# Kernel optimization log

Hardware: AMD Instinct MI355X
Metric: run time of the kernel (lower is better)

The kernel has to match this reference:

```python
import jax, jax.numpy as jnp
import numpy as np
import itertools

DIM = 7
N_H2, N_H3 = 21, 77

def _perm_sign(p):
    inv = sum(1 for i in range(len(p)) for j in range(i + 1, len(p)) if p[i] > p[j])
    return -1.0 if inv % 2 else 1.0

def _build_wedge_constants():
    # C[a,b,c] = sign of (pair_a, pair_b, triple_c) as a permutation of (0..6),
    # zero unless the 2+2+3 indices are disjoint (coefficient of the volume form
    # in omega_a ^ omega_b ^ Phi_c on ordered-multi-index components).
    idx2 = list(itertools.combinations(range(DIM), 2))   # 21 ordered pairs
    idx3 = list(itertools.combinations(range(DIM), 3))   # 35 ordered triples
    C = np.zeros((len(idx2), len(idx2), len(idx3)), dtype=np.float32)
    for a, pa in enumerate(idx2):
        sa = set(pa)
        for b, pb in enumerate(idx2):
            if sa & set(pb):
                continue
            sab = sa | set(pb)
            for c, pc in enumerate(idx3):
                full = pa + pb + pc
                if sab.isdisjoint(pc):
                    C[a, b, c] = _perm_sign(full)
    return jnp.asarray(C)

C_WEDGE = _build_wedge_constants()  # (21, 21, 35), sparse structure constants

def setup_inputs() -> dict:
    key = jax.random.key(0)
    k1, k2, k3 = jax.random.split(key, 3)
    batch = 4096
    omega = jax.random.normal(k1, (batch, N_H2, 21), dtype=jnp.float32)
    Phi = jax.random.normal(k2, (batch, N_H3, 35), dtype=jnp.float32)
    metric = jax.random.normal(k3, (batch, DIM, DIM), dtype=jnp.float32)
    return {"omega": omega, "Phi": Phi, "metric": metric}

def reference(omega, Phi, metric):
    # Monte-Carlo volume weights, normalized (normalize=True path)
    vol = jnp.sqrt(jnp.abs(jnp.linalg.det(metric)))        # (n,)
    w = vol / vol.sum()
    # Fused triple wedge contraction replacing the 21*21*77 python loops:
    # D[n,i,j,c] = sum_{a,b} C[a,b,c] omega[n,i,a] omega[n,j,b]
    D = jnp.einsum('abc,nia,njb->nijc', C_WEDGE, omega, omega)
    Pw = Phi * w[:, None, None]                             # fold MC weight into Phi
    S = jnp.einsum('nijc,nkc->ijk', D, Pw)                  # (21,21,77), symmetric in i,j
    # Original code writes +integral for j>=i and forces -integral for j<i
    upper = jnp.triu(jnp.ones((N_H2, N_H2), dtype=bool))[:, :, None]
    Y = jnp.where(upper, S, -S)
    # Gram matrix and spectrum
    M = jnp.einsum('ijk,ijl->kl', Y, Y)                     # (77,77)
    eigenvalues = jnp.linalg.eigvalsh(M)[::-1]              # descending, like torch path
    return Y, M, eigenvalues
```

## Files before the change

kernel.cpp:

```cpp
#include <hip/hip_runtime.h>
#include <math.h>

#define NBATCH 4096
#define NH2 21
#define NK 77
#define NC 35
#define NIJ 441
#define Y_SIZE 33957
#define M_SIZE 5929
#define VOLOFF Y_SIZE
#define VSUM (Y_SIZE + 4096)
#define NPAIR 231
#define BLK 512
#define NPB 8
#define GRID_B (NBATCH / NPB)
#define EIGT 640

#define NSLOT 16
#define SLOT_STRIDE 17792
#define WS2OFF (NSLOT * SLOT_STRIDE)

#define SZ_OMEGA  (NBATCH * NH2 * NH2)
#define SZ_PHI    (NBATCH * NK * NC)
#define SZ_METRIC (NBATCH * 7 * 7)

struct WTab {
  int a[NC][6];
  int b[NC][6];
  int sg[NC][6];
};

constexpr WTab make_wtab() {
  WTab W{};
  int p0[21] = {}, p1[21] = {};
  int idx = 0;
  for (int x = 0; x < 7; ++x)
    for (int y = x + 1; y < 7; ++y) { p0[idx] = x; p1[idx] = y; ++idx; }
  int t0[35] = {}, t1[35] = {}, t2[35] = {};
  idx = 0;
  for (int x = 0; x < 7; ++x)
    for (int y = x + 1; y < 7; ++y)
      for (int z = y + 1; z < 7; ++z) { t0[idx] = x; t1[idx] = y; t2[idx] = z; ++idx; }
  int cnt[35] = {};
  for (int a = 0; a < 21; ++a)
    for (int b = 0; b < 21; ++b) {
      int pa0 = p0[a], pa1 = p1[a], pb0 = p0[b], pb1 = p1[b];
      if (pa0 == pb0 || pa0 == pb1 || pa1 == pb0 || pa1 == pb1) continue;
      bool used[7] = {};
      used[pa0] = true; used[pa1] = true; used[pb0] = true; used[pb1] = true;
      int tr[3] = {}; int k = 0;
      for (int x = 0; x < 7; ++x) if (!used[x]) tr[k++] = x;
      int c = -1;
      for (int cc = 0; cc < 35; ++cc)
        if (t0[cc] == tr[0] && t1[cc] == tr[1] && t2[cc] == tr[2]) { c = cc; break; }
      int perm[7] = {pa0, pa1, pb0, pb1, tr[0], tr[1], tr[2]};
      int inv = 0;
      for (int i = 0; i < 7; ++i)
        for (int j = i + 1; j < 7; ++j)
          if (perm[i] > perm[j]) ++inv;
      W.a[c][cnt[c]] = a; W.b[c][cnt[c]] = b; W.sg[c][cnt[c]] = (inv & 1) ? -1 : 1;
      ++cnt[c];
    }
  return W;
}

__device__ __forceinline__ int trioff(int i) { return 21 * i - (i * (i - 1)) / 2; }

__device__ __forceinline__ unsigned f2bf(float x) {
  union { float f; unsigned u; } v; v.f = x;
  return ((v.u + 0x7FFFu + ((v.u >> 16) & 1u)) >> 16) & 0xFFFFu;
}

typedef float f32x4 __attribute__((ext_vector_type(4)));
typedef short s16x8 __attribute__((ext_vector_type(8)));

template <int CTRL>
__device__ __forceinline__ float dppadd(float x) {
  union { float f; int i; } u, r;
  u.f = x;
  r.i = __builtin_amdgcn_update_dpp(0, u.i, CTRL, 0xF, 0xF, true);
  return x + r.f;
}
__device__ __forceinline__ float oct_sum(float x) {
  x = dppadd<0xB1>(x);
  x = dppadd<0x4E>(x);
  x = dppadd<0x141>(x);
  return x;
}
__device__ __forceinline__ float wave_sum(float x) {
  x = dppadd<0xB1>(x);
  x = dppadd<0x4E>(x);
  x = dppadd<0x141>(x);
  x = dppadd<0x140>(x);
  x = dppadd<0x142>(x);
  x = dppadd<0x143>(x);
  return x;
}
__device__ __forceinline__ float readlane63(float x) {
  union { float f; int i; } u; u.f = x;
  union { int i; float f; } r;
  r.i = __builtin_amdgcn_readlane(u.i, 63);
  return r.f;
}

__global__ __launch_bounds__(256) void vol_kernel(const float* __restrict__ metric,
                                                  float* __restrict__ out) {
  const int n = blockIdx.x * 256 + threadIdx.x;
  double a[7][7];
#pragma unroll
  for (int r = 0; r < 7; ++r)
#pragma unroll
    for (int c = 0; c < 7; ++c) a[r][c] = (double)metric[n * 49 + r * 7 + c];

  double det = 1.0;
#pragma unroll
  for (int k = 0; k < 7; ++k) {
#pragma unroll
    for (int r = k + 1; r < 7; ++r) {
      bool sw = fabs(a[r][k]) > fabs(a[k][k]);
#pragma unroll
      for (int c = k; c < 7; ++c) {
        double u = a[k][c], v = a[r][c];
        a[k][c] = sw ? v : u;
        a[r][c] = sw ? u : v;
      }
    }
    det *= a[k][k];
    double inv = (a[k][k] != 0.0) ? 1.0 / a[k][k] : 0.0;
#pragma unroll
    for (int r = k + 1; r < 7; ++r) {
      double f = a[r][k] * inv;
#pragma unroll
      for (int c = k + 1; c < 7; ++c) a[r][c] -= f * a[k][c];
    }
  }
  float vol = (float)sqrt(fabs(det));
  out[VOLOFF + n] = vol;

  float s = vol;
#pragma unroll
  for (int off = 32; off > 0; off >>= 1) s += __shfl_down(s, off, 64);
  __shared__ float partial[4];
  const int lane = threadIdx.x & 63, wv = threadIdx.x >> 6;
  if (lane == 0) partial[wv] = s;
  __syncthreads();
  if (threadIdx.x == 0)
    atomicAdd(out + VSUM, partial[0] + partial[1] + partial[2] + partial[3]);
}

__global__ __launch_bounds__(BLK) void contract_kernel(const float* __restrict__ omega,
                                                       const float* __restrict__ Phi,
                                                       const float* __restrict__ out,
                                                       float* __restrict__ wsS) {
  constexpr WTab W = make_wtab();
  __shared__ __align__(16) short ldsD[256 * 80];
  __shared__ __align__(16) short ldsP[80 * 80];
  __shared__ __align__(16) float ldsO[NH2 * 28];

  const int t = threadIdx.x;
  const int lane = t & 63;
  const int wv = t >> 6;
  const int quad = lane >> 4;
  const int col = lane & 15;
  const int n0 = blockIdx.x * NPB;

  for (int f = t; f < 256 * 40; f += BLK) ((int*)ldsD)[f] = 0;
  for (int f = t; f < 80 * 40; f += BLK) ((int*)ldsP)[f] = 0;

  const bool roleA = (t < NPAIR);
  const bool roleB = (t >= 256) && (t < 256 + NPAIR);
  int pi = 0, pj = 0;
  {
    const int p = roleA ? t : (roleB ? (t - 256) : 0);
    int i = 0;
    while (i < 20 && trioff(i + 1) <= p) ++i;
    pi = i;
    pj = p - trioff(i) + i;
  }

  float rA = 0.0f, rB[6], rvn;
  {
    const float* om = omega + n0 * 441;
    const float* ph = Phi + n0 * 2695;
    if (t < 441) rA = om[t];
#pragma unroll
    for (int j = 0; j < 6; ++j) {
      const int e = t + j * BLK;
      rB[j] = (e < 2695) ? ph[e] : 0.0f;
    }
    rvn = out[VOLOFF + n0];
  }

  f32x4 acc[2][5];
#pragma unroll
  for (int mi = 0; mi < 2; ++mi)
#pragma unroll
    for (int nt = 0; nt < 5; ++nt) acc[mi][nt] = (f32x4){0.f, 0.f, 0.f, 0.f};

  for (int it = 0; it < NPB; ++it) {
    __syncthreads();

    if (t < 441) ldsO[(t / 21) * 28 + (t % 21)] = rA;
    {
      const float vn = rvn;
#pragma unroll
      for (int j = 0; j < 6; ++j) {
        const int e = t + j * BLK;
        if (e < 2695) {
          const int q = e / 35, c = e % 35;
          ldsP[q * 80 + c] = (short)f2bf(vn * rB[j]);
        }
      }
    }
    __syncthreads();

    if (it + 1 < NPB) {
      const int n1 = n0 + it + 1;
      const float* om2 = omega + n1 * 441;
      const float* ph2 = Phi + n1 * 2695;
      if (t < 441) rA = om2[t];
#pragma unroll
      for (int j = 0; j < 6; ++j) {
        const int e = t + j * BLK;
        if (e < 2695) rB[j] = ph2[e];
      }
      rvn = out[VOLOFF + n1];
    }

    if (roleA || roleB) {
      float wi[21], wj[21];
      const float* oi = ldsO + pi * 28;
      const float* oj = ldsO + pj * 28;
#pragma unroll
      for (int a = 0; a < 20; a += 4) {
        float4 v = *(const float4*)(oi + a);
        wi[a] = v.x; wi[a + 1] = v.y; wi[a + 2] = v.z; wi[a + 3] = v.w;
        float4 u = *(const float4*)(oj + a);
        wj[a] = u.x; wj[a + 1] = u.y; wj[a + 2] = u.z; wj[a + 3] = u.w;
      }
      wi[20] = oi[20]; wj[20] = oj[20];

      if (roleA) {
        float d[18];
#pragma unroll
        for (int c = 0; c < 18; ++c) {
          float dd = 0.0f;
#pragma unroll
          for (int u = 0; u < 6; ++u)
            dd = fmaf((W.sg[c][u] > 0) ? wi[W.a[c][u]] : -wi[W.a[c][u]], wj[W.b[c][u]], dd);
          d[c] = dd;
        }
        int* Drow = (int*)ldsD + t * 40;
#pragma unroll
        for (int k2 = 0; k2 < 9; ++k2)
          Drow[k2] = (int)(f2bf(d[2 * k2]) | (f2bf(d[2 * k2 + 1]) << 16));
      } else {
        float d[17];
#pragma unroll
        for (int c = 18; c < 35; ++c) {
          float dd = 0.0f;
#pragma unroll
          for (int u = 0; u < 6; ++u)
            dd = fmaf((W.sg[c][u] > 0) ? wi[W.a[c][u]] : -wi[W.a[c][u]], wj[W.b[c][u]], dd);
          d[c - 18] = dd;
        }
        int* Drow = (int*)ldsD + (t - 256) * 40;
#pragma unroll
        for (int k2 = 0; k2 < 8; ++k2)
          Drow[9 + k2] = (int)(f2bf(d[2 * k2]) | (f2bf(d[2 * k2 + 1]) << 16));
        Drow[17] = (int)f2bf(d[16]);
      }
    }
    __syncthreads();

#pragma unroll
    for (int s = 0; s < 2; ++s) {
      const int kof = s * 32 + quad * 8;
      s16x8 a0 = *(const s16x8*)(ldsD + ((wv * 2 + 0) * 16 + col) * 80 + kof);
      s16x8 a1 = *(const s16x8*)(ldsD + ((wv * 2 + 1) * 16 + col) * 80 + kof);
      s16x8 b[5];
#pragma unroll
      for (int nt = 0; nt < 5; ++nt)
        b[nt] = *(const s16x8*)(ldsP + (nt * 16 + col) * 80 + kof);
#pragma unroll
      for (int nt = 0; nt < 5; ++nt) {
        acc[0][nt] = __builtin_amdgcn_mfma_f32_16x16x32_bf16(a0, b[nt], acc[0][nt], 0, 0, 0);
        acc[1][nt] = __builtin_amdgcn_mfma_f32_16x16x32_bf16(a1, b[nt], acc[1][nt], 0, 0, 0);
      }
    }
  }

  float* slot = wsS + (size_t)(blockIdx.x & (NSLOT - 1)) * SLOT_STRIDE;
#pragma unroll
  for (int mi = 0; mi < 2; ++mi) {
    const int mt = wv * 2 + mi;
#pragma unroll
    for (int r = 0; r < 4; ++r) {
      const int m = mt * 16 + quad * 4 + r;
      if (m < NPAIR) {
#pragma unroll
        for (int nt = 0; nt < 5; ++nt) {
          const int q = nt * 16 + col;
          if (q < 77) atomicAdd(&slot[m * NK + q], acc[mi][nt][r]);
        }
      }
    }
  }
}

__global__ __launch_bounds__(256) void finalize_y(const float* __restrict__ wsS,
                                                  float* __restrict__ out) {
  const int e = blockIdx.x * 256 + threadIdx.x;
  if (e >= NPAIR * NK) return;
  const int p = e / NK, k = e % NK;
  int i = 0;
  while (i < 20 && trioff(i + 1) <= p) ++i;
  const int j = p - trioff(i) + i;
  float v = 0.0f;
#pragma unroll
  for (int s = 0; s < NSLOT; ++s) v += wsS[(size_t)s * SLOT_STRIDE + p * NK + k];
  v *= 1.0f / out[VSUM];
  out[(i * 21 + j) * NK + k] = v;
  if (j != i) out[(j * 21 + i) * NK + k] = -v;
}

__global__ __launch_bounds__(256) void gram_kernel(const float* __restrict__ Y,
                                                   float* __restrict__ Mout) {
  const int e = blockIdx.x * 256 + threadIdx.x;
  if (e >= M_SIZE) return;
  const int k = e / NK, l = e % NK;
  float acc = 0.0f;
  for (int ij = 0; ij < NIJ; ++ij)
    acc = fmaf(Y[ij * NK + k], Y[ij * NK + l], acc);
  Mout[e] = acc;
}

__global__ __launch_bounds__(64) void tridiag_kernel(const float* __restrict__ Min,
                                                     float* __restrict__ ws2) {
  const int l = threadIdx.x;
  const int br = l >> 3, bc = l & 7;
  float Areg[10][10];
#pragma unroll
  for (int r = 0; r < 10; ++r) {
    const int g = 10 * br + r;
#pragma unroll
    for (int c = 0; c < 10; ++c) {
      const int gc = 10 * bc + c;
      Areg[r][c] = (g < 77 && gc < 77) ? Min[g * 77 + gc] : 0.0f;
    }
  }

#pragma unroll 1
  for (int k = 0; k < 75; ++k) {
    const int kb = k / 10, ko = k % 10;
    float src[10];
#pragma unroll
    for (int rr = 0; rr < 10; ++rr)
      if (rr == ko) {
#pragma unroll
        for (int c = 0; c < 10; ++c) src[c] = Areg[rr][c];
      }
    const int idx_c = kb * 8 + bc;
    const int idx_r = kb * 8 + br;
    float rowk_c[10], rowk_r[10];
#pragma unroll
    for (int c = 0; c < 10; ++c) {
      rowk_c[c] = __shfl(src[c], idx_c, 64);
      rowk_r[c] = __shfl(src[c], idx_r, 64);
    }
    float part = 0.0f, xpart = 0.0f;
    if (br == 0) {
#pragma unroll
      for (int c = 0; c < 10; ++c) {
        const int gc = 10 * bc + c;
        const float x = rowk_c[c];
        part += (gc > k) ? x * x : 0.0f;
        xpart += (gc == k + 1) ? x : 0.0f;
      }
    }
    part = wave_sum(part);
    xpart = wave_sum(xpart);
    const float sigma2 = readlane63(part);
    if (sigma2 < 1e-26f) {
      if (l == 0) ws2[80 + k] = 0.0f;
      continue;
    }
    const float x1 = readlane63(xpart);
    const float sigma = sqrtf(sigma2);
    const float alpha = (x1 >= 0.0f) ? -sigma : sigma;
    const float beta = 1.0f / (sigma2 - alpha * x1);
    const float xha = x1 - alpha;
    if (l == 0) ws2[80 + k] = alpha;

    float vc[10], vr[10];
#pragma unroll
    for (int c = 0; c < 10; ++c) {
      const int gc = 10 * bc + c;
      vc[c] = (gc > k) ? ((gc == k + 1) ? xha : rowk_c[c]) : 0.0f;
      const int gr = 10 * br + c;
      vr[c] = (gr > k) ? ((gr == k + 1) ? xha : rowk_r[c]) : 0.0f;
    }

    float p[10];
#pragma unroll
    for (int r = 0; r < 10; ++r) {
      float s = 0.0f;
#pragma unroll
      for (int c = 0; c < 10; ++c) s = fmaf(Areg[r][c], vc[c], s);
      p[r] = s;
    }
#pragma unroll
    for (int r = 0; r < 10; ++r) {
      p[r] = oct_sum(p[r]) * beta;
      const int gr = 10 * br + r;
      p[r] = (gr > k) ? p[r] : 0.0f;
    }
    float kp = 0.0f;
    if (bc == 0) {
#pragma unroll
      for (int r = 0; r < 10; ++r) kp = fmaf(p[r], vr[r], kp);
    }
    kp = wave_sum(kp);
    const float K = readlane63(kp);
    const float hb = 0.5f * beta * K;

    float w[10];
#pragma unroll
    for (int r = 0; r < 10; ++r) w[r] = fmaf(-hb, vr[r], p[r]);
    const int idx_t = 9 * bc;
    float wc[10];
#pragma unroll
    for (int c = 0; c < 10; ++c) wc[c] = __shfl(w[c], idx_t, 64);

#pragma unroll
    for (int r = 0; r < 10; ++r)
#pragma unroll
      for (int c = 0; c < 10; ++c)
        Areg[r][c] -= vr[r] * wc[c] + w[r] * vc[c];
  }

  if (br == bc) {
#pragma unroll
    for (int e = 0; e < 10; ++e) ws2[10 * br + e] = Areg[e][e];
  }
  if (l == 63) ws2[80 + 75] = Areg[6][5];
}

__global__ __launch_bounds__(EIGT) void bisect_kernel(const float* __restrict__ ws2,
                                                      float* __restrict__ eout) {
  __shared__ float dsh[80], esh[80], e2sh[80];
  __shared__ float red[10], red2[10];
  const int t = threadIdx.x;
  const int lane = t & 63, wv = t >> 6;
  if (t < 80) {
    dsh[t] = ws2[t];
    esh[t] = (t < 76) ? ws2[80 + t] : 0.0f;
  }
  __syncthreads();
  if (t < 76) e2sh[t] = esh[t] * esh[t];

  float lo_ = 1e30f, hi_ = -1e30f;
  if (t < 77) {
    const float r = ((t > 0) ? fabsf(esh[t - 1]) : 0.0f) +
                    ((t < 76) ? fabsf(esh[t]) : 0.0f);
    lo_ = dsh[t] - r;
    hi_ = dsh[t] + r;
  }
#pragma unroll
  for (int off = 1; off < 64; off <<= 1) {
    lo_ = fminf(lo_, __shfl_xor(lo_, off, 64));
    hi_ = fmaxf(hi_, __shfl_xor(hi_, off, 64));
  }
  if (lane == 0) { red[wv] = lo_; red2[wv] = hi_; }
  __syncthreads();
  lo_ = red[0]; hi_ = red2[0];
#pragma unroll
  for (int u = 1; u < 10; ++u) { lo_ = fminf(lo_, red[u]); hi_ = fmaxf(hi_, red2[u]); }
  const float span = hi_ - lo_;
  const float glo = lo_ - 0.001f * span - 1e-6f;
  const float ghi = hi_ + 0.001f * span + 1e-6f;

  {
    const int e = t >> 3;
    const int s = t & 7;
    const int g = (t & 63) >> 3;
    float lo = glo, hi = ghi;
    for (int r = 0; r < 13; ++r) {
      const float step = (hi - lo) * (1.0f / 9.0f);
      const float x = fmaf(step, (float)(s + 1), lo);
      float q = dsh[0] - x;
      int cnt = (q < 0.0f);
#pragma unroll 4
      for (int i = 1; i < 77; ++i) {
        q = (fabsf(q) < 1e-30f) ? -1e-30f : q;
        q = dsh[i] - x - e2sh[i - 1] * __builtin_amdgcn_rcpf(q);
        cnt += (q < 0.0f);
      }
      const unsigned long long mask = __ballot(cnt > e);
      const int b = (int)((mask >> (g * 8)) & 0xFFull);
      const int z = b ? __builtin_ctz(b) : 8;
      const float nlo = fmaf(step, (float)z, lo);
      hi = (z == 8) ? hi : fmaf(step, (float)(z + 1), lo);
      lo = nlo;
    }
    if (s == 0 && e < 77) eout[76 - e] = 0.5f * (lo + hi);
  }
}

extern "C" void kernel_launch(void* const* d_in, const int* in_sizes, int n_in,
                              void* d_out, int out_size, void* d_ws, size_t ws_size,
                              hipStream_t stream) {
  const float* omega  = (const float*)d_in[0];
  const float* Phi    = (const float*)d_in[1];
  const float* metric = (const float*)d_in[2];
  for (int q = 0; q < n_in && q < 3; ++q) {
    if (in_sizes[q] == SZ_OMEGA)       omega  = (const float*)d_in[q];
    else if (in_sizes[q] == SZ_PHI)    Phi    = (const float*)d_in[q];
    else if (in_sizes[q] == SZ_METRIC) metric = (const float*)d_in[q];
  }

  float* out = (float*)d_out;
  float* ws  = (float*)d_ws;

  hipMemsetAsync(d_out, 0, (size_t)out_size * sizeof(float), stream);
  hipMemsetAsync(d_ws, 0, (size_t)WS2OFF * sizeof(float), stream);

  hipLaunchKernelGGL(vol_kernel, dim3(NBATCH / 256), dim3(256), 0, stream, metric, out);
  hipLaunchKernelGGL(contract_kernel, dim3(GRID_B), dim3(BLK), 0, stream,
                     omega, Phi, out, ws);
  hipLaunchKernelGGL(finalize_y, dim3((NPAIR * NK + 255) / 256), dim3(256), 0, stream,
                     ws, out);
  hipLaunchKernelGGL(gram_kernel, dim3((M_SIZE + 255) / 256), dim3(256), 0, stream,
                     out, out + Y_SIZE);
  hipLaunchKernelGGL(tridiag_kernel, dim3(1), dim3(64), 0, stream,
                     out + Y_SIZE, ws + WS2OFF);
  hipLaunchKernelGGL(bisect_kernel, dim3(1), dim3(EIGT), 0, stream,
                     ws + WS2OFF, out + Y_SIZE + M_SIZE);
}
```

Baseline: 379.5 us.

## Split gram reduction across lanes and pack tridiagonalization FMAs

The gram kernel now launches one block per row k with eight lanes sharing each (k,l) dot product, combined by an octet DPP reduction. This spreads the 441-term serial loop over more threads. The single-wave Householder tridiagonalization unrolls the inner row loop so the pivot row is read with a compile-time index instead of a predicated select. It also uses packed v_pk_fma_f32 for the matvec and rank-2 update, and derives vr by shuffle from vc. The added risks are register pressure in the fully unrolled loop and inline-asm scheduling constraints.

```diff
diff --git a/kernel.cpp b/kernel.cpp
--- a/kernel.cpp
+++ b/kernel.cpp
@@ -72,7 +72,14 @@
 }
 
 typedef float f32x4 __attribute__((ext_vector_type(4)));
+typedef float f32x2 __attribute__((ext_vector_type(2)));
 typedef short s16x8 __attribute__((ext_vector_type(8)));
+
+__device__ __forceinline__ f32x2 pk_fma(f32x2 a, f32x2 b, f32x2 c) {
+  f32x2 d;
+  asm volatile("v_pk_fma_f32 %0, %1, %2, %3" : "=v"(d) : "v"(a), "v"(b), "v"(c));
+  return d;
+}
 
 template <int CTRL>
 __device__ __forceinline__ float dppadd(float x) {
@@ -324,126 +331,141 @@
   if (j != i) out[(j * 21 + i) * NK + k] = -v;
 }
 
-__global__ __launch_bounds__(256) void gram_kernel(const float* __restrict__ Y,
-                                                   float* __restrict__ Mout) {
-  const int e = blockIdx.x * 256 + threadIdx.x;
-  if (e >= M_SIZE) return;
-  const int k = e / NK, l = e % NK;
+__global__ __launch_bounds__(EIGT) void gram_kernel(const float* __restrict__ Y,
+                                                    float* __restrict__ Mout) {
+  const int k = blockIdx.x;
+  const int t = threadIdx.x;
+  const int l = t >> 3, s = t & 7;
   float acc = 0.0f;
-  for (int ij = 0; ij < NIJ; ++ij)
-    acc = fmaf(Y[ij * NK + k], Y[ij * NK + l], acc);
-  Mout[e] = acc;
-}
-
-__global__ __launch_bounds__(64) void tridiag_kernel(const float* __restrict__ Min,
-                                                     float* __restrict__ ws2) {
+  if (l < NK) {
+    for (int ij = s; ij < NIJ; ij += 8)
+      acc = fmaf(Y[ij * NK + k], Y[ij * NK + l], acc);
+  }
+  acc = oct_sum(acc);
+  if (s == 0 && l < NK) Mout[k * NK + l] = acc;
+}
+
+__global__ __launch_bounds__(64, 1) void tridiag_kernel(const float* __restrict__ Min,
+                                                        float* __restrict__ ws2) {
   const int l = threadIdx.x;
   const int br = l >> 3, bc = l & 7;
-  float Areg[10][10];
+  f32x2 A2[10][5];
 #pragma unroll
   for (int r = 0; r < 10; ++r) {
     const int g = 10 * br + r;
 #pragma unroll
-    for (int c = 0; c < 10; ++c) {
-      const int gc = 10 * bc + c;
-      Areg[r][c] = (g < 77 && gc < 77) ? Min[g * 77 + gc] : 0.0f;
+    for (int c2 = 0; c2 < 5; ++c2) {
+      const int gc0 = 10 * bc + 2 * c2;
+      A2[r][c2][0] = (g < 77 && gc0 < 77) ? Min[g * 77 + gc0] : 0.0f;
+      A2[r][c2][1] = (g < 77 && gc0 + 1 < 77) ? Min[g * 77 + gc0 + 1] : 0.0f;
     }
   }
 
 #pragma unroll 1
-  for (int k = 0; k < 75; ++k) {
-    const int kb = k / 10, ko = k % 10;
-    float src[10];
-#pragma unroll
-    for (int rr = 0; rr < 10; ++rr)
-      if (rr == ko) {
-#pragma unroll
-        for (int c = 0; c < 10; ++c) src[c] = Areg[rr][c];
-      }
+  for (int kb = 0; kb < 8; ++kb) {
     const int idx_c = kb * 8 + bc;
-    const int idx_r = kb * 8 + br;
-    float rowk_c[10], rowk_r[10];
-#pragma unroll
-    for (int c = 0; c < 10; ++c) {
-      rowk_c[c] = __shfl(src[c], idx_c, 64);
-      rowk_r[c] = __shfl(src[c], idx_r, 64);
-    }
-    float part = 0.0f, xpart = 0.0f;
-    if (br == 0) {
-#pragma unroll
-      for (int c = 0; c < 10; ++c) {
-        const int gc = 10 * bc + c;
-        const float x = rowk_c[c];
-        part += (gc > k) ? x * x : 0.0f;
-        xpart += (gc == k + 1) ? x : 0.0f;
-      }
-    }
-    part = wave_sum(part);
-    xpart = wave_sum(xpart);
-    const float sigma2 = readlane63(part);
-    if (sigma2 < 1e-26f) {
-      if (l == 0) ws2[80 + k] = 0.0f;
-      continue;
-    }
-    const float x1 = readlane63(xpart);
-    const float sigma = sqrtf(sigma2);
-    const float alpha = (x1 >= 0.0f) ? -sigma : sigma;
-    const float beta = 1.0f / (sigma2 - alpha * x1);
-    const float xha = x1 - alpha;
-    if (l == 0) ws2[80 + k] = alpha;
-
-    float vc[10], vr[10];
-#pragma unroll
-    for (int c = 0; c < 10; ++c) {
-      const int gc = 10 * bc + c;
-      vc[c] = (gc > k) ? ((gc == k + 1) ? xha : rowk_c[c]) : 0.0f;
-      const int gr = 10 * br + c;
-      vr[c] = (gr > k) ? ((gr == k + 1) ? xha : rowk_r[c]) : 0.0f;
-    }
-
-    float p[10];
-#pragma unroll
-    for (int r = 0; r < 10; ++r) {
-      float s = 0.0f;
-#pragma unroll
-      for (int c = 0; c < 10; ++c) s = fmaf(Areg[r][c], vc[c], s);
-      p[r] = s;
-    }
-#pragma unroll
-    for (int r = 0; r < 10; ++r) {
-      p[r] = oct_sum(p[r]) * beta;
-      const int gr = 10 * br + r;
-      p[r] = (gr > k) ? p[r] : 0.0f;
-    }
-    float kp = 0.0f;
-    if (bc == 0) {
-#pragma unroll
-      for (int r = 0; r < 10; ++r) kp = fmaf(p[r], vr[r], kp);
-    }
-    kp = wave_sum(kp);
-    const float K = readlane63(kp);
-    const float hb = 0.5f * beta * K;
-
-    float w[10];
-#pragma unroll
-    for (int r = 0; r < 10; ++r) w[r] = fmaf(-hb, vr[r], p[r]);
-    const int idx_t = 9 * bc;
-    float wc[10];
-#pragma unroll
-    for (int c = 0; c < 10; ++c) wc[c] = __shfl(w[c], idx_t, 64);
-
-#pragma unroll
-    for (int r = 0; r < 10; ++r)
-#pragma unroll
-      for (int c = 0; c < 10; ++c)
-        Areg[r][c] -= vr[r] * wc[c] + w[r] * vc[c];
+#pragma unroll
+    for (int ko = 0; ko < 10; ++ko) {
+      if (kb == 7 && ko >= 5) break;
+      const int k = kb * 10 + ko;
+
+      f32x2 rowk2[5];
+#pragma unroll
+      for (int c2 = 0; c2 < 5; ++c2) {
+        rowk2[c2][0] = __shfl(A2[ko][c2][0], idx_c, 64);
+        rowk2[c2][1] = __shfl(A2[ko][c2][1], idx_c, 64);
+      }
+
+      float part = 0.0f, xpart = 0.0f;
+      if (br == 0) {
+#pragma unroll
+        for (int c2 = 0; c2 < 5; ++c2) {
+          const int gc0 = 10 * bc + 2 * c2;
+          const float x0 = rowk2[c2][0], x1v = rowk2[c2][1];
+          part += (gc0 > k) ? x0 * x0 : 0.0f;
+          part += (gc0 + 1 > k) ? x1v * x1v : 0.0f;
+          xpart += (gc0 == k + 1) ? x0 : 0.0f;
+          xpart += (gc0 + 1 == k + 1) ? x1v : 0.0f;
+        }
+      }
+      part = wave_sum(part);
+      xpart = wave_sum(xpart);
+      const float sigma2 = readlane63(part);
+      if (sigma2 < 1e-26f) {
+        if (l == 0) ws2[80 + k] = 0.0f;
+        continue;
+      }
+      const float x1 = readlane63(xpart);
+      const float sigma = sqrtf(sigma2);
+      const float alpha = (x1 >= 0.0f) ? -sigma : sigma;
+      const float beta = 1.0f / (sigma2 - alpha * x1);
+      const float xha = x1 - alpha;
+      if (l == 0) ws2[80 + k] = alpha;
+
+      f32x2 vc2[5];
+#pragma unroll
+      for (int c2 = 0; c2 < 5; ++c2) {
+        const int gc0 = 10 * bc + 2 * c2;
+        vc2[c2][0] = (gc0 > k) ? ((gc0 == k + 1) ? xha : rowk2[c2][0]) : 0.0f;
+        vc2[c2][1] = (gc0 + 1 > k) ? ((gc0 + 1 == k + 1) ? xha : rowk2[c2][1]) : 0.0f;
+      }
+      float vr[10];
+#pragma unroll
+      for (int c2 = 0; c2 < 5; ++c2) {
+        vr[2 * c2] = __shfl(vc2[c2][0], br, 64);
+        vr[2 * c2 + 1] = __shfl(vc2[c2][1], br, 64);
+      }
+
+      float p[10];
+#pragma unroll
+      for (int r = 0; r < 10; ++r) {
+        f32x2 a = (f32x2){0.f, 0.f};
+#pragma unroll
+        for (int c2 = 0; c2 < 5; ++c2) a = pk_fma(A2[r][c2], vc2[c2], a);
+        p[r] = a[0] + a[1];
+      }
+#pragma unroll
+      for (int r = 0; r < 10; ++r) {
+        p[r] = oct_sum(p[r]) * beta;
+        p[r] = (10 * br + r > k) ? p[r] : 0.0f;
+      }
+
+      float kp = 0.0f;
+      if (bc == 0) {
+#pragma unroll
+        for (int r = 0; r < 10; ++r) kp = fmaf(p[r], vr[r], kp);
+      }
+      kp = wave_sum(kp);
+      const float hb = 0.5f * beta * readlane63(kp);
+
+      float w[10];
+#pragma unroll
+      for (int r = 0; r < 10; ++r) w[r] = fmaf(-hb, vr[r], p[r]);
+      const int diag = 9 * bc;
+      f32x2 wc2[5];
+#pragma unroll
+      for (int c2 = 0; c2 < 5; ++c2) {
+        wc2[c2][0] = __shfl(w[2 * c2], diag, 64);
+        wc2[c2][1] = __shfl(w[2 * c2 + 1], diag, 64);
+      }
+
+#pragma unroll
+      for (int r = 0; r < 10; ++r) {
+        const f32x2 nv = (f32x2){-vr[r], -vr[r]};
+        const f32x2 nw = (f32x2){-w[r], -w[r]};
+#pragma unroll
+        for (int c2 = 0; c2 < 5; ++c2)
+          A2[r][c2] = pk_fma(nv, wc2[c2], pk_fma(nw, vc2[c2], A2[r][c2]));
+      }
+    }
   }
 
   if (br == bc) {
 #pragma unroll
-    for (int e = 0; e < 10; ++e) ws2[10 * br + e] = Areg[e][e];
-  }
-  if (l == 63) ws2[80 + 75] = Areg[6][5];
+    for (int e = 0; e < 10; ++e)
+      ws2[10 * br + e] = (e & 1) ? A2[e][e / 2][1] : A2[e][e / 2][0];
+  }
+  if (l == 63) ws2[80 + 75] = A2[6][2][1];
 }
 
 __global__ __launch_bounds__(EIGT) void bisect_kernel(const float* __restrict__ ws2,
@@ -530,7 +552,7 @@
                      omega, Phi, out, ws);
   hipLaunchKernelGGL(finalize_y, dim3((NPAIR * NK + 255) / 256), dim3(256), 0, stream,
                      ws, out);
-  hipLaunchKernelGGL(gram_kernel, dim3((M_SIZE + 255) / 256), dim3(256), 0, stream,
+  hipLaunchKernelGGL(gram_kernel, dim3(NK), dim3(EIGT), 0, stream,
                      out, out + Y_SIZE);
   hipLaunchKernelGGL(tridiag_kernel, dim3(1), dim3(64), 0, stream,
                      out + Y_SIZE, ws + WS2OFF);
```

Result: faster. 348.9 us (-8.1%).
